# Kernel optimization log

Measured on AMD Instinct MI355X. Metric: run time of the kernel, lower is better.

Reference implementation:

```python
import jax, jax.numpy as jnp
import numpy as np

D = 128   # embedding_dim
H = 256   # hidden_dim

def setup_inputs() -> dict:
    key = jax.random.key(0)
    ks = jax.random.split(key, 16)
    s = 0.02
    B, N = 4, 384
    inp = {
        "cities": jax.random.uniform(ks[0], (B, N, 2), dtype=jnp.float32),
        # city_encoder: Linear(2,H) -> ReLU -> Linear(H,D); weights stored [in,out]
        "We1": jax.random.normal(ks[1], (2, H), dtype=jnp.float32) * s,
        "be1": jnp.zeros((H,), jnp.float32),
        "We2": jax.random.normal(ks[2], (H, D), dtype=jnp.float32) * s,
        "be2": jnp.zeros((D,), jnp.float32),
        # attention: Linear(D,H) -> ReLU -> Linear(H,1)
        "Wa1": jax.random.normal(ks[3], (D, H), dtype=jnp.float32) * s,
        "ba1": jnp.zeros((H,), jnp.float32),
        "wa2": jax.random.normal(ks[4], (H, 1), dtype=jnp.float32) * s,
        "ba2": jnp.zeros((1,), jnp.float32),
        # decoder: Linear(2D,H) -> ReLU -> Linear(H,1) -> Sigmoid
        "Wd1": jax.random.normal(ks[5], (2 * D, H), dtype=jnp.float32) * s,
        "bd1": jnp.zeros((H,), jnp.float32),
        "wd2": jax.random.normal(ks[6], (H, 1), dtype=jnp.float32) * s,
        "bd2": jnp.zeros((1,), jnp.float32),
    }
    return inp


def reference(cities, We1, be1, We2, be2, Wa1, ba1, wa2, ba2, Wd1, bd1, wd2, bd2):
    B, N, _ = cities.shape
    # city encoder MLP: [B,N,2] -> [B,N,D]
    emb = jax.nn.relu(cities @ We1 + be1) @ We2 + be2
    # attention scores -> softmax over cities
    att = jax.nn.softmax((jax.nn.relu(emb @ Wa1 + ba1) @ wa2 + ba2).squeeze(-1), axis=1)
    # Pairwise decoder: concat(e_i, e_j) @ Wd1 == e_i @ Wd1[:D] + e_j @ Wd1[D:]
    Ai = emb @ Wd1[:D]   # [B,N,H] contribution of row city i
    Aj = emb @ Wd1[D:]   # [B,N,H] contribution of col city j
    h = jax.nn.relu(Ai[:, :, None, :] + Aj[:, None, :, :] + bd1)  # [B,N,N,H]
    p = jax.nn.sigmoid((h @ wd2).squeeze(-1) + bd2)               # [B,N,N]
    # diagonal (i == j) was never written in the torch loop -> stays 0
    p = p * (1.0 - jnp.eye(N, dtype=p.dtype))
    return att, p
```

## Files before the change

### kernel.cpp

```cpp
#include <hip/hip_runtime.h>
#include <hip/hip_fp16.h>
#include <math.h>

#define NCITY 384
#define BATCH 4
#define DIM   128
#define HID   256
#define M_TOT (BATCH * NCITY)
#define TR    3

#define HALF_FLOATS 8192

#define VMWAIT8()  do { asm volatile("s_waitcnt vmcnt(8)"  ::: "memory"); \
                        __builtin_amdgcn_sched_barrier(0); } while (0)
#define VMWAIT0()  do { asm volatile("s_waitcnt vmcnt(0)"  ::: "memory"); \
                        __builtin_amdgcn_sched_barrier(0); } while (0)
#define LGKM0()    do { asm volatile("s_waitcnt lgkmcnt(0)" ::: "memory"); \
                        __builtin_amdgcn_sched_barrier(0); } while (0)
#define SBAR()     do { __builtin_amdgcn_s_barrier(); \
                        __builtin_amdgcn_sched_barrier(0); } while (0)

__device__ __forceinline__ void stage32(const float* __restrict__ gsrc,
                                        float* lbuf, int tid)
{
    const int lane = tid & 63;
    const int wv   = tid >> 6;
    #pragma unroll
    for (int i = 0; i < 8; ++i) {
        const int slot = i * 4 + wv;
        __builtin_amdgcn_global_load_lds(
            (const __attribute__((address_space(1))) void*)(gsrc + slot * 256 + lane * 4),
            (__attribute__((address_space(3))) void*)(lbuf + slot * 256),
            16, 0, 0);
    }
}

__device__ __forceinline__ void emb_half(const float* buf,
                                         const float (*h1_s)[HID],
                                         int tid, int kbase, float4 eacc[TR])
{
    const int d4 = tid & 31;
    const int k0 = (tid >> 5) * 8;
    #pragma unroll
    for (int kb = 0; kb < 8; kb += 4) {
        float4 hv[TR];
        #pragma unroll
        for (int rr = 0; rr < TR; ++rr)
            hv[rr] = *(const float4*)&h1_s[rr][kbase + k0 + kb];
        #pragma unroll
        for (int kk = 0; kk < 4; ++kk) {
            const float4 w4 = *(const float4*)&buf[(k0 + kb + kk) * DIM + d4 * 4];
            #pragma unroll
            for (int rr = 0; rr < TR; ++rr) {
                const float h = ((const float*)&hv[rr])[kk];
                eacc[rr].x = fmaf(h, w4.x, eacc[rr].x);
                eacc[rr].y = fmaf(h, w4.y, eacc[rr].y);
                eacc[rr].z = fmaf(h, w4.z, eacc[rr].z);
                eacc[rr].w = fmaf(h, w4.w, eacc[rr].w);
            }
        }
    }
}

__device__ __forceinline__ void chunk_half(const float* buf,
                                           const float (*emb_s)[DIM],
                                           int tid, int kbase, float4 cacc[TR])
{
    const int c4 = tid & 63;
    const int k0 = (tid >> 6) * 8;
    #pragma unroll
    for (int kb = 0; kb < 8; kb += 4) {
        float4 ev[TR];
        #pragma unroll
        for (int rr = 0; rr < TR; ++rr)
            ev[rr] = *(const float4*)&emb_s[rr][kbase + k0 + kb];
        #pragma unroll
        for (int kk = 0; kk < 4; ++kk) {
            const float4 w4 = *(const float4*)&buf[(k0 + kb + kk) * HID + c4 * 4];
            #pragma unroll
            for (int rr = 0; rr < TR; ++rr) {
                const float e = ((const float*)&ev[rr])[kk];
                cacc[rr].x = fmaf(e, w4.x, cacc[rr].x);
                cacc[rr].y = fmaf(e, w4.y, cacc[rr].y);
                cacc[rr].z = fmaf(e, w4.z, cacc[rr].z);
                cacc[rr].w = fmaf(e, w4.w, cacc[rr].w);
            }
        }
    }
}

__device__ __forceinline__ void chunk_reduce(float* scr, int tid,
                                             const float4 cacc[TR], float out6[TR])
{
    const int c4 = tid & 63;
    const int wv = tid >> 6;
    SBAR();
    #pragma unroll
    for (int rr = 0; rr < TR; ++rr)
        *(float4*)&scr[(wv * TR + rr) * HID + c4 * 4] = cacc[rr];
    LGKM0(); SBAR();
    #pragma unroll
    for (int rr = 0; rr < TR; ++rr)
        out6[rr] = scr[(0 * TR + rr) * HID + tid] + scr[(1 * TR + rr) * HID + tid]
                 + scr[(2 * TR + rr) * HID + tid] + scr[(3 * TR + rr) * HID + tid];
}

__global__ __launch_bounds__(256) void encoder_kernel(
    const float* __restrict__ cities,
    const float* __restrict__ We1, const float* __restrict__ be1,
    const float* __restrict__ We2, const float* __restrict__ be2,
    const float* __restrict__ Wa1, const float* __restrict__ ba1,
    const float* __restrict__ wa2, const float* __restrict__ ba2,
    const float* __restrict__ Wd1, const float* __restrict__ bd1,
    float* __restrict__ score, float* __restrict__ Ai, float* __restrict__ Aj)
{
    __shared__ float wbuf[2 * HALF_FLOATS];
    __shared__ float h1_s[TR][HID];
    __shared__ float emb_s[TR][DIM];
    __shared__ float red2[4][TR];

    float* b0 = wbuf;
    float* b1 = wbuf + HALF_FLOATS;

    const int tid = threadIdx.x;
    const int r0  = blockIdx.x * TR;

    const float w0 = We1[tid], w1 = We1[HID + tid], bb1 = be1[tid];
    const float ba1v = ba1[tid], wa2v = wa2[tid], bd1v = bd1[tid];
    const float be2v = be2[tid & (DIM - 1)];
    float cx[TR], cy[TR];
    #pragma unroll
    for (int rr = 0; rr < TR; ++rr) {
        cx[rr] = cities[(r0 + rr) * 2];
        cy[rr] = cities[(r0 + rr) * 2 + 1];
    }
    #pragma unroll
    for (int rr = 0; rr < TR; ++rr)
        h1_s[rr][tid] = fmaxf(fmaf(cx[rr], w0, fmaf(cy[rr], w1, bb1)), 0.f);
    __builtin_amdgcn_sched_barrier(0);

    float4 eacc[TR];
    #pragma unroll
    for (int rr = 0; rr < TR; ++rr) eacc[rr] = make_float4(0.f, 0.f, 0.f, 0.f);

    stage32(We2,                   b0, tid);
    stage32(We2 + 1 * HALF_FLOATS, b1, tid);
    VMWAIT8(); LGKM0(); SBAR();
    emb_half(b0, h1_s, tid, 0, eacc);
    SBAR();
    stage32(We2 + 2 * HALF_FLOATS, b0, tid);
    VMWAIT8(); SBAR();
    emb_half(b1, h1_s, tid, 64, eacc);
    SBAR();
    stage32(We2 + 3 * HALF_FLOATS, b1, tid);
    VMWAIT8(); SBAR();
    emb_half(b0, h1_s, tid, 128, eacc);
    SBAR();
    stage32(Wa1, b0, tid);
    VMWAIT8(); SBAR();
    emb_half(b1, h1_s, tid, 192, eacc);

    {
        #pragma unroll
        for (int rr = 0; rr < TR; ++rr) {
            eacc[rr].x += __shfl_xor(eacc[rr].x, 32);
            eacc[rr].y += __shfl_xor(eacc[rr].y, 32);
            eacc[rr].z += __shfl_xor(eacc[rr].z, 32);
            eacc[rr].w += __shfl_xor(eacc[rr].w, 32);
        }
        SBAR();
        if ((tid & 63) < 32) {
            const int wv = tid >> 6, d4 = tid & 31;
            #pragma unroll
            for (int rr = 0; rr < TR; ++rr)
                *(float4*)&b1[(wv * TR + rr) * DIM + d4 * 4] = eacc[rr];
        }
        LGKM0(); SBAR();
        #pragma unroll
        for (int j = 0; j < 2; ++j) {
            const int o = tid + j * 256;
            if (o < TR * DIM) {
                const int rr = o >> 7, d = o & (DIM - 1);
                emb_s[rr][d] = b1[(0 * TR + rr) * DIM + d] + b1[(1 * TR + rr) * DIM + d]
                             + b1[(2 * TR + rr) * DIM + d] + b1[(3 * TR + rr) * DIM + d]
                             + be2v;
            }
        }
        LGKM0(); SBAR();
    }

    float4 cacc[TR];
    float o6[TR];

    stage32(Wa1 + 1 * HALF_FLOATS, b1, tid);
    VMWAIT8(); SBAR();
    #pragma unroll
    for (int rr = 0; rr < TR; ++rr) cacc[rr] = make_float4(0.f, 0.f, 0.f, 0.f);
    chunk_half(b0, emb_s, tid, 0, cacc);
    SBAR();
    stage32(Wa1 + 2 * HALF_FLOATS, b0, tid);
    VMWAIT8(); SBAR();
    chunk_half(b1, emb_s, tid, 32, cacc);
    SBAR();
    stage32(Wa1 + 3 * HALF_FLOATS, b1, tid);
    VMWAIT8(); SBAR();
    chunk_half(b0, emb_s, tid, 64, cacc);
    SBAR();
    stage32(Wd1, b0, tid);
    VMWAIT8(); SBAR();
    chunk_half(b1, emb_s, tid, 96, cacc);
    chunk_reduce(b1, tid, cacc, o6);
    {
        const int wv = tid >> 6;
        #pragma unroll
        for (int rr = 0; rr < TR; ++rr) {
            float v = fmaxf(o6[rr] + ba1v, 0.f) * wa2v;
            #pragma unroll
            for (int off = 32; off > 0; off >>= 1)
                v += __shfl_down(v, off);
            if ((tid & 63) == 0) red2[wv][rr] = v;
        }
        LGKM0(); SBAR();
        if (tid < TR)
            score[r0 + tid] = red2[0][tid] + red2[1][tid] + red2[2][tid] + red2[3][tid];
    }

    stage32(Wd1 + 1 * HALF_FLOATS, b1, tid);
    VMWAIT8(); SBAR();
    #pragma unroll
    for (int rr = 0; rr < TR; ++rr) cacc[rr] = make_float4(0.f, 0.f, 0.f, 0.f);
    chunk_half(b0, emb_s, tid, 0, cacc);
    SBAR();
    stage32(Wd1 + 2 * HALF_FLOATS, b0, tid);
    VMWAIT8(); SBAR();
    chunk_half(b1, emb_s, tid, 32, cacc);
    SBAR();
    stage32(Wd1 + 3 * HALF_FLOATS, b1, tid);
    VMWAIT8(); SBAR();
    chunk_half(b0, emb_s, tid, 64, cacc);
    SBAR();
    stage32(Wd1 + 4 * HALF_FLOATS, b0, tid);
    VMWAIT8(); SBAR();
    chunk_half(b1, emb_s, tid, 96, cacc);
    chunk_reduce(b1, tid, cacc, o6);
    #pragma unroll
    for (int rr = 0; rr < TR; ++rr)
        Ai[(r0 + rr) * HID + tid] = o6[rr] + bd1v;
    SBAR();

    stage32(Wd1 + 5 * HALF_FLOATS, b1, tid);
    VMWAIT8(); SBAR();
    #pragma unroll
    for (int rr = 0; rr < TR; ++rr) cacc[rr] = make_float4(0.f, 0.f, 0.f, 0.f);
    chunk_half(b0, emb_s, tid, 0, cacc);
    SBAR();
    stage32(Wd1 + 6 * HALF_FLOATS, b0, tid);
    VMWAIT8(); SBAR();
    chunk_half(b1, emb_s, tid, 32, cacc);
    SBAR();
    stage32(Wd1 + 7 * HALF_FLOATS, b1, tid);
    VMWAIT8(); SBAR();
    chunk_half(b0, emb_s, tid, 64, cacc);
    VMWAIT0(); SBAR();
    chunk_half(b1, emb_s, tid, 96, cacc);
    chunk_reduce(b0, tid, cacc, o6);
    #pragma unroll
    for (int rr = 0; rr < TR; ++rr)
        Aj[(r0 + rr) * HID + tid] = o6[rr];
    (void)ba2;
}

__device__ __forceinline__ unsigned pk_add(unsigned a, unsigned b) {
    unsigned r;
    asm("v_pk_add_f16 %0, %1, %2" : "=v"(r) : "v"(a), "v"(b));
    return r;
}
__device__ __forceinline__ unsigned pk_max0(unsigned a) {
    unsigned r;
    asm("v_pk_max_f16 %0, %1, %2" : "=v"(r) : "v"(a), "v"(0u));
    return r;
}
__device__ __forceinline__ unsigned pk_fma(unsigned a, unsigned b, unsigned c) {
    unsigned r;
    asm("v_pk_fma_f16 %0, %1, %2, %3" : "=v"(r) : "v"(a), "v"(b), "v"(c));
    return r;
}
__device__ __forceinline__ unsigned pack2(float a, float b) {
    union { __half2 h2; unsigned u; } c;
    c.h2 = __float22half2_rn(make_float2(a, b));
    return c.u;
}
__device__ __forceinline__ float sum2(unsigned u) {
    union { unsigned u; __half2 h2; } c;
    c.u = u;
    return __low2float(c.h2) + __high2float(c.h2);
}

union H8 { float4 f4; unsigned u[4]; };

__global__ __launch_bounds__(256) void pair_sm_kernel(
    const float* __restrict__ Ai, const float* __restrict__ Aj,
    const float* __restrict__ wd2, const float* __restrict__ bd2,
    const float* __restrict__ score, float* __restrict__ att,
    float* __restrict__ p)
{
    const int tid = threadIdx.x;
    const int b   = blockIdx.y;

    if (blockIdx.x == 144) {
        __shared__ float red[8];
        const int t = tid;
        const float v0 = score[b * NCITY + t];
        const bool  h2v = (t < NCITY - 256);
        const float v1 = h2v ? score[b * NCITY + 256 + t] : -3.4e38f;
        float m = fmaxf(v0, v1);
        #pragma unroll
        for (int off = 32; off > 0; off >>= 1)
            m = fmaxf(m, __shfl_down(m, off));
        if ((t & 63) == 0) red[t >> 6] = m;
        __syncthreads();
        m = fmaxf(fmaxf(red[0], red[1]), fmaxf(red[2], red[3]));
        const float e0 = __expf(v0 - m);
        const float e1 = h2v ? __expf(v1 - m) : 0.f;
        float s = e0 + e1;
        #pragma unroll
        for (int off = 32; off > 0; off >>= 1)
            s += __shfl_down(s, off);
        if ((t & 63) == 0) red[4 + (t >> 6)] = s;
        __syncthreads();
        s = red[4] + red[5] + red[6] + red[7];
        att[b * NCITY + t] = e0 / s;
        if (h2v) att[b * NCITY + 256 + t] = e1 / s;
        return;
    }

    __shared__ __half ai_s[32 * HID];
    __shared__ __half aj_s[32 * HID];
    __shared__ unsigned wd2h[HID / 2];

    const int i0 = (blockIdx.x / 12) * 32;
    const int j0 = (blockIdx.x % 12) * 32;

    if (tid < HID / 2) {
        const float2 w2 = *(const float2*)&wd2[tid * 2];
        wd2h[tid] = pack2(w2.x, w2.y);
    }

    for (int u = tid; u < 32 * 32; u += 256) {
        const int r = u >> 5, s = u & 31;
        const int su = (s ^ (r & 15)) * 8;
        {
            const int g = (b * NCITY + i0 + r) * HID + s * 8;
            const float4 f0 = *(const float4*)&Ai[g];
            const float4 f1 = *(const float4*)&Ai[g + 4];
            H8 pk;
            pk.u[0] = pack2(f0.x, f0.y);
            pk.u[1] = pack2(f0.z, f0.w);
            pk.u[2] = pack2(f1.x, f1.y);
            pk.u[3] = pack2(f1.z, f1.w);
            *(float4*)&ai_s[r * HID + su] = pk.f4;
        }
        {
            const int g = (b * NCITY + j0 + r) * HID + s * 8;
            const float4 f0 = *(const float4*)&Aj[g];
            const float4 f1 = *(const float4*)&Aj[g + 4];
            H8 pk;
            pk.u[0] = pack2(f0.x, f0.y);
            pk.u[1] = pack2(f0.z, f0.w);
            pk.u[2] = pack2(f1.x, f1.y);
            pk.u[3] = pack2(f1.z, f1.w);
            *(float4*)&aj_s[r * HID + su] = pk.f4;
        }
    }
    __syncthreads();

    const int tx = tid & 15;
    const int ty = tid >> 4;

    unsigned a00A = 0u, a00B = 0u, a01A = 0u, a01B = 0u;
    unsigned a10A = 0u, a10B = 0u, a11A = 0u, a11B = 0u;

    #pragma unroll 4
    for (int k8 = 0; k8 < 32; ++k8) {
        const int ci = (k8 ^ ty) * 8;
        const int cj = (k8 ^ tx) * 8;
        H8 x0, x1, y0, y1;
        x0.f4 = *(const float4*)&ai_s[ ty       * HID + ci];
        x1.f4 = *(const float4*)&ai_s[(ty + 16) * HID + ci];
        y0.f4 = *(const float4*)&aj_s[ tx       * HID + cj];
        y1.f4 = *(const float4*)&aj_s[(tx + 16) * HID + cj];

        #pragma unroll
        for (int q = 0; q < 4; ++q) {
            const unsigned w = wd2h[k8 * 4 + q];
            const unsigned t00 = pk_max0(pk_add(x0.u[q], y0.u[q]));
            const unsigned t01 = pk_max0(pk_add(x0.u[q], y1.u[q]));
            const unsigned t10 = pk_max0(pk_add(x1.u[q], y0.u[q]));
            const unsigned t11 = pk_max0(pk_add(x1.u[q], y1.u[q]));
            if (q < 2) {
                a00A = pk_fma(t00, w, a00A);
                a01A = pk_fma(t01, w, a01A);
                a10A = pk_fma(t10, w, a10A);
                a11A = pk_fma(t11, w, a11A);
            } else {
                a00B = pk_fma(t00, w, a00B);
                a01B = pk_fma(t01, w, a01B);
                a10B = pk_fma(t10, w, a10B);
                a11B = pk_fma(t11, w, a11B);
            }
        }
    }

    const float bd = bd2[0];
    float accs[2][2];
    accs[0][0] = sum2(a00A) + sum2(a00B);
    accs[0][1] = sum2(a01A) + sum2(a01B);
    accs[1][0] = sum2(a10A) + sum2(a10B);
    accs[1][1] = sum2(a11A) + sum2(a11B);

    #pragma unroll
    for (int ii = 0; ii < 2; ++ii) {
        #pragma unroll
        for (int jj = 0; jj < 2; ++jj) {
            const int gi = i0 + ty + ii * 16;
            const int gj = j0 + tx + jj * 16;
            const float v = 1.f / (1.f + __expf(-(accs[ii][jj] + bd)));
            p[(b * NCITY + gi) * NCITY + gj] = (gi == gj) ? 0.f : v;
        }
    }
}

extern "C" void kernel_launch(void* const* d_in, const int* in_sizes, int n_in,
                              void* d_out, int out_size, void* d_ws, size_t ws_size,
                              hipStream_t stream)
{
    const float* cities = (const float*)d_in[0];
    const float* We1    = (const float*)d_in[1];
    const float* be1    = (const float*)d_in[2];
    const float* We2    = (const float*)d_in[3];
    const float* be2    = (const float*)d_in[4];
    const float* Wa1    = (const float*)d_in[5];
    const float* ba1    = (const float*)d_in[6];
    const float* wa2    = (const float*)d_in[7];
    const float* ba2    = (const float*)d_in[8];
    const float* Wd1    = (const float*)d_in[9];
    const float* bd1    = (const float*)d_in[10];
    const float* wd2    = (const float*)d_in[11];
    const float* bd2    = (const float*)d_in[12];

    float* out_att = (float*)d_out;
    float* out_p   = out_att + BATCH * NCITY;

    float* score = (float*)d_ws;
    float* Ai    = score + M_TOT;
    float* Aj    = Ai + M_TOT * HID;

    encoder_kernel<<<M_TOT / TR, 256, 0, stream>>>(
        cities, We1, be1, We2, be2, Wa1, ba1, wa2, ba2, Wd1, bd1,
        score, Ai, Aj);

    pair_sm_kernel<<<dim3(145, BATCH), 256, 0, stream>>>(
        Ai, Aj, wd2, bd2, score, out_att, out_p);
}
```

Baseline: 37.92 us.

## Fuse encoder and pairwise decoder into one persistent kernel with flag sync

Merges the encoder and pair/softmax kernels into a single launch of 384 blocks. Each block first encodes 4 rows and publishes a per-block magic flag, then picks up pair tiles and softmax tasks, spinning on the flags of the rows it needs. Ai/Aj are now stored as fp16, which halves the intermediate traffic and drops the repacking in the pair stage. The goal is to remove the second launch and the gap between kernels. In exchange it adds spin-wait cross-block dependencies that assume all producer blocks are co-resident, and magic flags left in the workspace could look valid on a later call if the workspace is not cleared.

```diff
diff --git a/kernel.cpp b/kernel.cpp
--- a/kernel.cpp
+++ b/kernel.cpp
@@ -1,15 +1,16 @@
 #include <hip/hip_runtime.h>
 #include <hip/hip_fp16.h>
-#include <math.h>
 
 #define NCITY 384
 #define BATCH 4
 #define DIM   128
 #define HID   256
 #define M_TOT (BATCH * NCITY)
-#define TR    3
-
+#define TR    4
+#define NBLK  (M_TOT / TR)
+#define NTASK (576 + BATCH)
 #define HALF_FLOATS 8192
+#define MAGIC 0x5A5AC3C3D2D24B4BULL
 
 #define VMWAIT8()  do { asm volatile("s_waitcnt vmcnt(8)"  ::: "memory"); \
                         __builtin_amdgcn_sched_barrier(0); } while (0)
@@ -20,6 +21,26 @@
 #define SBAR()     do { __builtin_amdgcn_s_barrier(); \
                         __builtin_amdgcn_sched_barrier(0); } while (0)
 
+__device__ __forceinline__ unsigned pk_add(unsigned a, unsigned b) {
+    unsigned r; asm("v_pk_add_f16 %0, %1, %2" : "=v"(r) : "v"(a), "v"(b)); return r;
+}
+__device__ __forceinline__ unsigned pk_max0(unsigned a) {
+    unsigned r; asm("v_pk_max_f16 %0, %1, %2" : "=v"(r) : "v"(a), "v"(0u)); return r;
+}
+__device__ __forceinline__ unsigned pk_fma(unsigned a, unsigned b, unsigned c) {
+    unsigned r; asm("v_pk_fma_f16 %0, %1, %2, %3" : "=v"(r) : "v"(a), "v"(b), "v"(c)); return r;
+}
+__device__ __forceinline__ unsigned pack2(float a, float b) {
+    union { __half2 h2; unsigned u; } c;
+    c.h2 = __float22half2_rn(make_float2(a, b));
+    return c.u;
+}
+__device__ __forceinline__ float sum2(unsigned u) {
+    union { unsigned u; __half2 h2; } c; c.u = u;
+    return __low2float(c.h2) + __high2float(c.h2);
+}
+union H8 { float4 f4; unsigned u[4]; };
+
 __device__ __forceinline__ void stage32(const float* __restrict__ gsrc,
                                         float* lbuf, int tid)
 {
@@ -105,14 +126,17 @@
                  + scr[(2 * TR + rr) * HID + tid] + scr[(3 * TR + rr) * HID + tid];
 }
 
-__global__ __launch_bounds__(256) void encoder_kernel(
+__global__ __launch_bounds__(256) void fused_kernel(
     const float* __restrict__ cities,
     const float* __restrict__ We1, const float* __restrict__ be1,
     const float* __restrict__ We2, const float* __restrict__ be2,
     const float* __restrict__ Wa1, const float* __restrict__ ba1,
     const float* __restrict__ wa2, const float* __restrict__ ba2,
     const float* __restrict__ Wd1, const float* __restrict__ bd1,
-    float* __restrict__ score, float* __restrict__ Ai, float* __restrict__ Aj)
+    const float* __restrict__ wd2, const float* __restrict__ bd2,
+    float* __restrict__ score, __half* __restrict__ Ai_h, __half* __restrict__ Aj_h,
+    unsigned long long* __restrict__ flags,
+    float* __restrict__ att, float* __restrict__ p)
 {
     __shared__ float wbuf[2 * HALF_FLOATS];
     __shared__ float h1_s[TR][HID];
@@ -123,7 +147,8 @@
     float* b1 = wbuf + HALF_FLOATS;
 
     const int tid = threadIdx.x;
-    const int r0  = blockIdx.x * TR;
+    const int bid = blockIdx.x;
+    const int r0  = bid * TR;
 
     const float w0 = We1[tid], w1 = We1[HID + tid], bb1 = be1[tid];
     const float ba1v = ba1[tid], wa2v = wa2[tid], bd1v = bd1[tid];
@@ -179,12 +204,10 @@
         #pragma unroll
         for (int j = 0; j < 2; ++j) {
             const int o = tid + j * 256;
-            if (o < TR * DIM) {
-                const int rr = o >> 7, d = o & (DIM - 1);
-                emb_s[rr][d] = b1[(0 * TR + rr) * DIM + d] + b1[(1 * TR + rr) * DIM + d]
-                             + b1[(2 * TR + rr) * DIM + d] + b1[(3 * TR + rr) * DIM + d]
-                             + be2v;
-            }
+            const int rr = o >> 7, d = o & (DIM - 1);
+            emb_s[rr][d] = b1[(0 * TR + rr) * DIM + d] + b1[(1 * TR + rr) * DIM + d]
+                         + b1[(2 * TR + rr) * DIM + d] + b1[(3 * TR + rr) * DIM + d]
+                         + be2v;
         }
         LGKM0(); SBAR();
     }
@@ -245,7 +268,7 @@
     chunk_reduce(b1, tid, cacc, o6);
     #pragma unroll
     for (int rr = 0; rr < TR; ++rr)
-        Ai[(r0 + rr) * HID + tid] = o6[rr] + bd1v;
+        Ai_h[(r0 + rr) * HID + tid] = __float2half(o6[rr] + bd1v);
     SBAR();
 
     stage32(Wd1 + 5 * HALF_FLOATS, b1, tid);
@@ -266,166 +289,139 @@
     chunk_reduce(b0, tid, cacc, o6);
     #pragma unroll
     for (int rr = 0; rr < TR; ++rr)
-        Aj[(r0 + rr) * HID + tid] = o6[rr];
+        Aj_h[(r0 + rr) * HID + tid] = __float2half(o6[rr]);
     (void)ba2;
-}
-
-__device__ __forceinline__ unsigned pk_add(unsigned a, unsigned b) {
-    unsigned r;
-    asm("v_pk_add_f16 %0, %1, %2" : "=v"(r) : "v"(a), "v"(b));
-    return r;
-}
-__device__ __forceinline__ unsigned pk_max0(unsigned a) {
-    unsigned r;
-    asm("v_pk_max_f16 %0, %1, %2" : "=v"(r) : "v"(a), "v"(0u));
-    return r;
-}
-__device__ __forceinline__ unsigned pk_fma(unsigned a, unsigned b, unsigned c) {
-    unsigned r;
-    asm("v_pk_fma_f16 %0, %1, %2, %3" : "=v"(r) : "v"(a), "v"(b), "v"(c));
-    return r;
-}
-__device__ __forceinline__ unsigned pack2(float a, float b) {
-    union { __half2 h2; unsigned u; } c;
-    c.h2 = __float22half2_rn(make_float2(a, b));
-    return c.u;
-}
-__device__ __forceinline__ float sum2(unsigned u) {
-    union { unsigned u; __half2 h2; } c;
-    c.u = u;
-    return __low2float(c.h2) + __high2float(c.h2);
-}
-
-union H8 { float4 f4; unsigned u[4]; };
-
-__global__ __launch_bounds__(256) void pair_sm_kernel(
-    const float* __restrict__ Ai, const float* __restrict__ Aj,
-    const float* __restrict__ wd2, const float* __restrict__ bd2,
-    const float* __restrict__ score, float* __restrict__ att,
-    float* __restrict__ p)
-{
-    const int tid = threadIdx.x;
-    const int b   = blockIdx.y;
-
-    if (blockIdx.x == 144) {
-        __shared__ float red[8];
-        const int t = tid;
-        const float v0 = score[b * NCITY + t];
-        const bool  h2v = (t < NCITY - 256);
-        const float v1 = h2v ? score[b * NCITY + 256 + t] : -3.4e38f;
-        float m = fmaxf(v0, v1);
-        #pragma unroll
-        for (int off = 32; off > 0; off >>= 1)
-            m = fmaxf(m, __shfl_down(m, off));
-        if ((t & 63) == 0) red[t >> 6] = m;
+
+    __threadfence();
+    __syncthreads();
+    if (tid == 0)
+        __hip_atomic_store(&flags[bid], MAGIC, __ATOMIC_RELAXED,
+                           __HIP_MEMORY_SCOPE_AGENT);
+
+    const float bd = bd2[0];
+    __half*   ai_s = (__half*)wbuf;
+    __half*   aj_s = (__half*)wbuf + 32 * HID;
+    unsigned* wd2h = (unsigned*)(wbuf + 8192);
+
+    for (int t = bid; t < NTASK; t += NBLK) {
         __syncthreads();
-        m = fmaxf(fmaxf(red[0], red[1]), fmaxf(red[2], red[3]));
-        const float e0 = __expf(v0 - m);
-        const float e1 = h2v ? __expf(v1 - m) : 0.f;
-        float s = e0 + e1;
-        #pragma unroll
-        for (int off = 32; off > 0; off >>= 1)
-            s += __shfl_down(s, off);
-        if ((t & 63) == 0) red[4 + (t >> 6)] = s;
-        __syncthreads();
-        s = red[4] + red[5] + red[6] + red[7];
-        att[b * NCITY + t] = e0 / s;
-        if (h2v) att[b * NCITY + 256 + t] = e1 / s;
-        return;
-    }
-
-    __shared__ __half ai_s[32 * HID];
-    __shared__ __half aj_s[32 * HID];
-    __shared__ unsigned wd2h[HID / 2];
-
-    const int i0 = (blockIdx.x / 12) * 32;
-    const int j0 = (blockIdx.x % 12) * 32;
-
-    if (tid < HID / 2) {
-        const float2 w2 = *(const float2*)&wd2[tid * 2];
-        wd2h[tid] = pack2(w2.x, w2.y);
-    }
-
-    for (int u = tid; u < 32 * 32; u += 256) {
-        const int r = u >> 5, s = u & 31;
-        const int su = (s ^ (r & 15)) * 8;
-        {
-            const int g = (b * NCITY + i0 + r) * HID + s * 8;
-            const float4 f0 = *(const float4*)&Ai[g];
-            const float4 f1 = *(const float4*)&Ai[g + 4];
-            H8 pk;
-            pk.u[0] = pack2(f0.x, f0.y);
-            pk.u[1] = pack2(f0.z, f0.w);
-            pk.u[2] = pack2(f1.x, f1.y);
-            pk.u[3] = pack2(f1.z, f1.w);
-            *(float4*)&ai_s[r * HID + su] = pk.f4;
-        }
-        {
-            const int g = (b * NCITY + j0 + r) * HID + s * 8;
-            const float4 f0 = *(const float4*)&Aj[g];
-            const float4 f1 = *(const float4*)&Aj[g + 4];
-            H8 pk;
-            pk.u[0] = pack2(f0.x, f0.y);
-            pk.u[1] = pack2(f0.z, f0.w);
-            pk.u[2] = pack2(f1.x, f1.y);
-            pk.u[3] = pack2(f1.z, f1.w);
-            *(float4*)&aj_s[r * HID + su] = pk.f4;
-        }
-    }
-    __syncthreads();
-
-    const int tx = tid & 15;
-    const int ty = tid >> 4;
-
-    unsigned a00A = 0u, a00B = 0u, a01A = 0u, a01B = 0u;
-    unsigned a10A = 0u, a10B = 0u, a11A = 0u, a11B = 0u;
-
-    #pragma unroll 4
-    for (int k8 = 0; k8 < 32; ++k8) {
-        const int ci = (k8 ^ ty) * 8;
-        const int cj = (k8 ^ tx) * 8;
-        H8 x0, x1, y0, y1;
-        x0.f4 = *(const float4*)&ai_s[ ty       * HID + ci];
-        x1.f4 = *(const float4*)&ai_s[(ty + 16) * HID + ci];
-        y0.f4 = *(const float4*)&aj_s[ tx       * HID + cj];
-        y1.f4 = *(const float4*)&aj_s[(tx + 16) * HID + cj];
-
-        #pragma unroll
-        for (int q = 0; q < 4; ++q) {
-            const unsigned w = wd2h[k8 * 4 + q];
-            const unsigned t00 = pk_max0(pk_add(x0.u[q], y0.u[q]));
-            const unsigned t01 = pk_max0(pk_add(x0.u[q], y1.u[q]));
-            const unsigned t10 = pk_max0(pk_add(x1.u[q], y0.u[q]));
-            const unsigned t11 = pk_max0(pk_add(x1.u[q], y1.u[q]));
-            if (q < 2) {
-                a00A = pk_fma(t00, w, a00A);
-                a01A = pk_fma(t01, w, a01A);
-                a10A = pk_fma(t10, w, a10A);
-                a11A = pk_fma(t11, w, a11A);
-            } else {
-                a00B = pk_fma(t00, w, a00B);
-                a01B = pk_fma(t01, w, a01B);
-                a10B = pk_fma(t10, w, a10B);
-                a11B = pk_fma(t11, w, a11B);
-            }
-        }
-    }
-
-    const float bd = bd2[0];
-    float accs[2][2];
-    accs[0][0] = sum2(a00A) + sum2(a00B);
-    accs[0][1] = sum2(a01A) + sum2(a01B);
-    accs[1][0] = sum2(a10A) + sum2(a10B);
-    accs[1][1] = sum2(a11A) + sum2(a11B);
-
-    #pragma unroll
-    for (int ii = 0; ii < 2; ++ii) {
-        #pragma unroll
-        for (int jj = 0; jj < 2; ++jj) {
-            const int gi = i0 + ty + ii * 16;
-            const int gj = j0 + tx + jj * 16;
-            const float v = 1.f / (1.f + __expf(-(accs[ii][jj] + bd)));
-            p[(b * NCITY + gi) * NCITY + gj] = (gi == gj) ? 0.f : v;
+        if (t < 576) {
+            const int b   = t / 144;
+            const int rem = t % 144;
+            const int i0  = (rem / 12) * 32;
+            const int j0  = (rem % 12) * 32;
+
+            if (tid < 8) {
+                const unsigned long long* f = &flags[(b * NCITY + i0) / TR + tid];
+                while (__hip_atomic_load(f, __ATOMIC_RELAXED,
+                                         __HIP_MEMORY_SCOPE_AGENT) != MAGIC) {}
+            } else if (tid < 16) {
+                const unsigned long long* f = &flags[(b * NCITY + j0) / TR + (tid - 8)];
+                while (__hip_atomic_load(f, __ATOMIC_RELAXED,
+                                         __HIP_MEMORY_SCOPE_AGENT) != MAGIC) {}
+            }
+            __threadfence();
+            __syncthreads();
+
+            if (tid < HID / 2) {
+                const float2 w2 = *(const float2*)&wd2[tid * 2];
+                wd2h[tid] = pack2(w2.x, w2.y);
+            }
+            for (int u = tid; u < 32 * 32; u += 256) {
+                const int r = u >> 5, s = u & 31;
+                const int su = (s ^ (r & 15)) * 8;
+                *(float4*)&ai_s[r * HID + su] =
+                    *(const float4*)&Ai_h[(b * NCITY + i0 + r) * HID + s * 8];
+                *(float4*)&aj_s[r * HID + su] =
+                    *(const float4*)&Aj_h[(b * NCITY + j0 + r) * HID + s * 8];
+            }
+            __syncthreads();
+
+            const int tx = tid & 15;
+            const int ty = tid >> 4;
+
+            unsigned a00A = 0u, a00B = 0u, a01A = 0u, a01B = 0u;
+            unsigned a10A = 0u, a10B = 0u, a11A = 0u, a11B = 0u;
+
+            #pragma unroll 4
+            for (int k8 = 0; k8 < 32; ++k8) {
+                const int ci = (k8 ^ ty) * 8;
+                const int cj = (k8 ^ tx) * 8;
+                H8 x0, x1, y0, y1;
+                x0.f4 = *(const float4*)&ai_s[ ty       * HID + ci];
+                x1.f4 = *(const float4*)&ai_s[(ty + 16) * HID + ci];
+                y0.f4 = *(const float4*)&aj_s[ tx       * HID + cj];
+                y1.f4 = *(const float4*)&aj_s[(tx + 16) * HID + cj];
+
+                #pragma unroll
+                for (int q = 0; q < 4; ++q) {
+                    const unsigned w = wd2h[k8 * 4 + q];
+                    const unsigned t00 = pk_max0(pk_add(x0.u[q], y0.u[q]));
+                    const unsigned t01 = pk_max0(pk_add(x0.u[q], y1.u[q]));
+                    const unsigned t10 = pk_max0(pk_add(x1.u[q], y0.u[q]));
+                    const unsigned t11 = pk_max0(pk_add(x1.u[q], y1.u[q]));
+                    if (q < 2) {
+                        a00A = pk_fma(t00, w, a00A);
+                        a01A = pk_fma(t01, w, a01A);
+                        a10A = pk_fma(t10, w, a10A);
+                        a11A = pk_fma(t11, w, a11A);
+                    } else {
+                        a00B = pk_fma(t00, w, a00B);
+                        a01B = pk_fma(t01, w, a01B);
+                        a10B = pk_fma(t10, w, a10B);
+                        a11B = pk_fma(t11, w, a11B);
+                    }
+                }
+            }
+
+            float accs[2][2];
+            accs[0][0] = sum2(a00A) + sum2(a00B);
+            accs[0][1] = sum2(a01A) + sum2(a01B);
+            accs[1][0] = sum2(a10A) + sum2(a10B);
+            accs[1][1] = sum2(a11A) + sum2(a11B);
+
+            #pragma unroll
+            for (int ii = 0; ii < 2; ++ii) {
+                #pragma unroll
+                for (int jj = 0; jj < 2; ++jj) {
+                    const int gi = i0 + ty + ii * 16;
+                    const int gj = j0 + tx + jj * 16;
+                    const float v = 1.f / (1.f + __expf(-(accs[ii][jj] + bd)));
+                    p[(b * NCITY + gi) * NCITY + gj] = (gi == gj) ? 0.f : v;
+                }
+            }
+        } else {
+            const int bb = t - 576;
+            if (tid < 96) {
+                const unsigned long long* f = &flags[bb * 96 + tid];
+                while (__hip_atomic_load(f, __ATOMIC_RELAXED,
+                                         __HIP_MEMORY_SCOPE_AGENT) != MAGIC) {}
+            }
+            __threadfence();
+            __syncthreads();
+
+            float* red = wbuf;
+            const float v0 = score[bb * NCITY + tid];
+            const bool  h2v = (tid < NCITY - 256);
+            const float v1 = h2v ? score[bb * NCITY + 256 + tid] : -3.4e38f;
+            float m = fmaxf(v0, v1);
+            #pragma unroll
+            for (int off = 32; off > 0; off >>= 1)
+                m = fmaxf(m, __shfl_down(m, off));
+            if ((tid & 63) == 0) red[tid >> 6] = m;
+            __syncthreads();
+            m = fmaxf(fmaxf(red[0], red[1]), fmaxf(red[2], red[3]));
+            const float e0 = __expf(v0 - m);
+            const float e1 = h2v ? __expf(v1 - m) : 0.f;
+            float s = e0 + e1;
+            #pragma unroll
+            for (int off = 32; off > 0; off >>= 1)
+                s += __shfl_down(s, off);
+            if ((tid & 63) == 0) red[4 + (tid >> 6)] = s;
+            __syncthreads();
+            s = red[4] + red[5] + red[6] + red[7];
+            att[bb * NCITY + tid] = e0 / s;
+            if (h2v) att[bb * NCITY + 256 + tid] = e1 / s;
         }
     }
 }
@@ -449,16 +445,14 @@
     const float* bd2    = (const float*)d_in[12];
 
     float* out_att = (float*)d_out;
-    float* out_p   = out_att + BATCH * NCITY;
-
-    float* score = (float*)d_ws;
-    float* Ai    = score + M_TOT;
-    float* Aj    = Ai + M_TOT * HID;
-
-    encoder_kernel<<<M_TOT / TR, 256, 0, stream>>>(
-        cities, We1, be1, We2, be2, Wa1, ba1, wa2, ba2, Wd1, bd1,
-        score, Ai, Aj);
-
-    pair_sm_kernel<<<dim3(145, BATCH), 256, 0, stream>>>(
-        Ai, Aj, wd2, bd2, score, out_att, out_p);
-}
+    float* out_p   = out_att + M_TOT;
+
+    float*  score = (float*)d_ws;
+    __half* Ai_h  = (__half*)(score + M_TOT);
+    __half* Aj_h  = Ai_h + M_TOT * HID;
+    unsigned long long* flags = (unsigned long long*)(Aj_h + M_TOT * HID);
+
+    fused_kernel<<<NBLK, 256, 0, stream>>>(
+        cities, We1, be1, We2, be2, Wa1, ba1, wa2, ba2, Wd1, bd1, wd2, bd2,
+        score, Ai_h, Aj_h, flags, out_att, out_p);
+}
```

Result: slower. 117.8 us (+210.7%).
